# Optimization experiments

Measured on AMD Instinct MI355X. Metric: run time of the kernel, lower is better.

Reference implementation:

```python
import jax, jax.numpy as jnp
import numpy as np
from jax import lax

# BatchNorm2d(affine=False) in eval mode with initial running stats (mean=0, var=1)
# reduces to a constant scale. (Original torch module in train mode would use batch
# stats of the dispatched subset; we use the eval-mode form for a deterministic,
# vectorizable reference.)
BN_SCALE = 1.0 / np.sqrt(1.0 + 1e-5)
DN = ('NCHW', 'OIHW', 'NCHW')


def _dw(x, w, pad, dil=1):
    # depthwise conv, kernel [C,1,k,k]
    return lax.conv_general_dilated(x, w, (1, 1), [(pad, pad), (pad, pad)],
                                    rhs_dilation=(dil, dil), dimension_numbers=DN,
                                    feature_group_count=x.shape[1])


def _pw(x, w):
    # pointwise 1x1 conv, kernel [C,C,1,1]
    return lax.conv_general_dilated(x, w, (1, 1), 'VALID', dimension_numbers=DN)


def _sep(x, d1, p1, d2, p2, pad):
    # DARTS SepConv: (ReLU-dw-pw-BN) x 2
    y = _pw(_dw(jax.nn.relu(x), d1, pad), p1) * BN_SCALE
    return _pw(_dw(jax.nn.relu(y), d2, pad), p2) * BN_SCALE


def _dil(x, d, p, pad):
    # DARTS DilConv: ReLU-dw(dilation=2)-pw-BN
    return _pw(_dw(jax.nn.relu(x), d, pad, 2), p) * BN_SCALE


def _maxpool3(x):
    y = jnp.pad(x, ((0, 0), (0, 0), (1, 1), (1, 1)), constant_values=-jnp.inf)
    return lax.reduce_window(y, -jnp.inf, lax.max, (1, 1, 3, 3), (1, 1, 1, 1), 'VALID')


def _avgpool3(x):
    # avg_pool 3x3 stride 1 pad 1, count_include_pad=False
    pad = [(0, 0), (0, 0), (1, 1), (1, 1)]
    s = lax.reduce_window(x, 0.0, lax.add, (1, 1, 3, 3), (1, 1, 1, 1), pad)
    c = lax.reduce_window(jnp.ones_like(x), 0.0, lax.add, (1, 1, 3, 3), (1, 1, 1, 1), pad)
    return s / c


def _mixed_forward(x, weights, params, top):
    B, n_op = weights.shape
    _, idx = lax.top_k(weights, top)                    # [B, top]
    sel = jax.nn.one_hot(idx, n_op).sum(axis=1) > 0     # [B, n_op] bool: op in top-k
    # softmax over logits masked to -inf outside top-k => non-selected ops weight 0
    gate = jax.nn.softmax(jnp.where(sel, weights, -jnp.inf), axis=-1)  # [B, n_op]
    (sc3_d1, sc3_p1, sc3_d2, sc3_p2,
     sc5_d1, sc5_p1, sc5_d2, sc5_p2,
     dc3_d, dc3_p, dc5_d, dc5_p) = params
    # PRIMITIVES order: none, max_pool_3x3, avg_pool_3x3, skip_connect,
    # sep_conv_3x3, sep_conv_5x5, dil_conv_3x3, dil_conv_5x5
    op_outs = [
        None,                        # 'none' contributes zeros
        _maxpool3(x) * BN_SCALE,     # pool ops are followed by BN(affine=False)
        _avgpool3(x) * BN_SCALE,
        x,                           # skip_connect (stride=1 -> Identity)
        _sep(x, sc3_d1, sc3_p1, sc3_d2, sc3_p2, 1),
        _sep(x, sc5_d1, sc5_p1, sc5_d2, sc5_p2, 2),
        _dil(x, dc3_d, dc3_p, 2),
        _dil(x, dc5_d, dc5_p, 4),
    ]
    out = jnp.zeros_like(x)
    for i, y in enumerate(op_outs):
        if y is not None:
            out = out + gate[:, i, None, None, None] * y
    return out, weights  # second output is gate_value_cp (clone of gate input)


def setup_inputs():
    key = jax.random.key(0)
    ks = jax.random.split(key, 16)
    B, C, H, W = 64, 128, 32, 32
    def p(k, shape):
        return jax.random.normal(k, shape, jnp.float32) * 0.05
    return {
        'x': jax.random.normal(ks[0], (B, C, H, W), jnp.float32),
        'weights': jax.random.normal(ks[1], (B, 8), jnp.float32),
        'sc3_d1': p(ks[2], (C, 1, 3, 3)), 'sc3_p1': p(ks[3], (C, C, 1, 1)),
        'sc3_d2': p(ks[4], (C, 1, 3, 3)), 'sc3_p2': p(ks[5], (C, C, 1, 1)),
        'sc5_d1': p(ks[6], (C, 1, 5, 5)), 'sc5_p1': p(ks[7], (C, C, 1, 1)),
        'sc5_d2': p(ks[8], (C, 1, 5, 5)), 'sc5_p2': p(ks[9], (C, C, 1, 1)),
        'dc3_d': p(ks[10], (C, 1, 3, 3)), 'dc3_p': p(ks[11], (C, C, 1, 1)),
        'dc5_d': p(ks[12], (C, 1, 5, 5)), 'dc5_p': p(ks[13], (C, C, 1, 1)),
        'top': 2,
    }


def reference(x, weights, sc3_d1, sc3_p1, sc3_d2, sc3_p2, sc5_d1, sc5_p1, sc5_d2, sc5_p2, dc3_d, dc3_p, dc5_d, dc5_p, top):
    params = (sc3_d1, sc3_p1, sc3_d2, sc3_p2, sc5_d1, sc5_p1, sc5_d2, sc5_p2,
              dc3_d, dc3_p, dc5_d, dc5_p)
    return _mixed_forward(x, weights, params, top)
```

## Files before the change

### kernel.cpp

```cpp
#include <hip/hip_runtime.h>
#include <hip/hip_bf16.h>


#define BN_SCALE 0.9999950000374997f
#define BB 64
#define CC 128
#define HH 32
#define WW 32
#define PLANE (HH*WW)
#define SAMP (CC*PLANE)
#define NOUT0 (BB*SAMP)
#define LROW 136

typedef __attribute__((ext_vector_type(8))) short bf16x8;
typedef __attribute__((ext_vector_type(4))) float f32x4;

__device__ __forceinline__ float us2f(unsigned int u) {
    unsigned int x = (u & 0xffffu) << 16;
    float f; __builtin_memcpy(&f, &x, 4); return f;
}
__device__ __forceinline__ unsigned short f2us(float f) {
    __hip_bfloat16 h = __float2bfloat16(f);
    unsigned short u; __builtin_memcpy(&u, &h, 2); return u;
}

__global__ void k_gates(const float* __restrict__ wlog,
                        const void* __restrict__ topp,
                        float* __restrict__ gates,
                        int* __restrict__ cnum, int* __restrict__ cops,
                        float* __restrict__ out_w) {
    int b = threadIdx.x;

    int top = -1;
    {
        unsigned int u0 = *(const unsigned int*)topp;
        int i32 = (int)u0;
        if (i32 >= 1 && i32 <= 8) top = i32;
        else {
            float f32; __builtin_memcpy(&f32, &u0, 4);
            if (f32 >= 1.f && f32 <= 8.f) top = (int)(f32 + 0.5f);
            else { float fb = us2f(u0); if (fb >= 1.f && fb <= 8.f) top = (int)(fb + 0.5f); }
        }
        if (top < 1 || top > 8) top = 2;
    }

    float lw[8];
    #pragma unroll
    for (int i = 0; i < 8; ++i) {
        lw[i] = wlog[b * 8 + i];
        out_w[b * 8 + i] = lw[i];
    }
    bool sel[8] = {false,false,false,false,false,false,false,false};
    for (int t = 0; t < top; ++t) {
        int best = -1; float bv = -3.4e38f;
        #pragma unroll
        for (int i = 0; i < 8; ++i)
            if (!sel[i] && lw[i] > bv) { bv = lw[i]; best = i; }
        if (best >= 0) sel[best] = true;
    }
    float m = -3.4e38f;
    #pragma unroll
    for (int i = 0; i < 8; ++i) if (sel[i] && lw[i] > m) m = lw[i];
    float s = 0.f, e[8];
    #pragma unroll
    for (int i = 0; i < 8; ++i) { e[i] = sel[i] ? expf(lw[i] - m) : 0.f; s += e[i]; }
    float inv = (s > 0.f) ? 1.f / s : 0.f;
    float g[8];
    #pragma unroll
    for (int i = 0; i < 8; ++i) {
        g[i] = (s > 0.f) ? e[i] * inv : (sel[i] ? 1.f / (float)top : 0.f);
        gates[b * 8 + i] = g[i];
    }
    int n = 0;
    #pragma unroll
    for (int i = 4; i < 8; ++i)
        if (g[i] > 0.f) { if (n < 4) cops[b * 4 + n] = i; ++n; }
    cnum[b] = (n < 4) ? n : 4;
}

__global__ __launch_bounds__(256) void
k_pools(const float* __restrict__ x,
        const float* __restrict__ gates,
        float* __restrict__ out) {
    int plane = blockIdx.x;
    int b = plane >> 7;
    float g1 = gates[b * 8 + 1] * BN_SCALE;
    float g2 = gates[b * 8 + 2] * BN_SCALE;
    float g3 = gates[b * 8 + 3];
    float* op = out + (size_t)plane * PLANE;
    if (g1 == 0.f && g2 == 0.f && g3 == 0.f) {
        ((float4*)op)[threadIdx.x] = make_float4(0.f, 0.f, 0.f, 0.f);
        return;
    }
    __shared__ float sx[PLANE];
    ((float4*)sx)[threadIdx.x] = ((const float4*)(x + (size_t)plane * PLANE))[threadIdx.x];
    __syncthreads();
    #pragma unroll
    for (int j = 0; j < 4; ++j) {
        int px = threadIdx.x + j * 256;
        int h = px >> 5, w = px & 31;
        float mx = -3.4e38f, sm = 0.f;
        int cnt = 0;
        #pragma unroll
        for (int dh = -1; dh <= 1; ++dh) {
            int ih = h + dh;
            if ((unsigned)ih >= HH) continue;
            #pragma unroll
            for (int dw = -1; dw <= 1; ++dw) {
                int iw = w + dw;
                if ((unsigned)iw >= WW) continue;
                float v = sx[ih * WW + iw];
                mx = fmaxf(mx, v);
                sm += v;
                ++cnt;
            }
        }
        op[px] = g1 * mx + g2 * (sm / (float)cnt) + g3 * sx[px];
    }
}

template <int K, int DIL>
__device__ __forceinline__ void dw_comp(const float* __restrict__ sx,
                                        const float* __restrict__ wd, int c,
                                        unsigned short* __restrict__ opp) {
    constexpr int PAD = (K / 2) * DIL;
    float wk[K * K];
    #pragma unroll
    for (int i = 0; i < K * K; ++i) wk[i] = wd[c * K * K + i];
    #pragma unroll
    for (int j = 0; j < 4; ++j) {
        int px = threadIdx.x + j * 256;
        int h = px >> 5, w = px & 31;
        float acc = 0.f;
        #pragma unroll
        for (int ky = 0; ky < K; ++ky) {
            int ih = h + ky * DIL - PAD;
            if ((unsigned)ih >= HH) continue;
            #pragma unroll
            for (int kx = 0; kx < K; ++kx) {
                int iw = w + kx * DIL - PAD;
                if ((unsigned)iw >= WW) continue;
                acc = fmaf(wk[ky * K + kx], sx[ih * WW + iw], acc);
            }
        }
        opp[px] = f2us(acc);
    }
}

__global__ __launch_bounds__(256) void
k_dw_first(const float* __restrict__ x,
           const float* __restrict__ w4, const float* __restrict__ w5,
           const float* __restrict__ w6, const float* __restrict__ w7,
           const float* __restrict__ gates,
           unsigned short* __restrict__ A4, unsigned short* __restrict__ A5,
           unsigned short* __restrict__ P6, unsigned short* __restrict__ P7) {
    int plane = blockIdx.x;
    int b = plane >> 7, c = plane & 127;
    float g4 = gates[b * 8 + 4], g5 = gates[b * 8 + 5];
    float g6 = gates[b * 8 + 6], g7 = gates[b * 8 + 7];
    if (g4 == 0.f && g5 == 0.f && g6 == 0.f && g7 == 0.f) return;
    __shared__ float sx[PLANE];
    {
        float4 v = ((const float4*)(x + (size_t)plane * PLANE))[threadIdx.x];
        ((float4*)sx)[threadIdx.x] =
            make_float4(fmaxf(v.x, 0.f), fmaxf(v.y, 0.f),
                        fmaxf(v.z, 0.f), fmaxf(v.w, 0.f));
    }
    __syncthreads();
    size_t off = (size_t)plane * PLANE;
    if (g4 != 0.f) dw_comp<3, 1>(sx, w4, c, A4 + off);
    if (g5 != 0.f) dw_comp<5, 1>(sx, w5, c, A5 + off);
    if (g6 != 0.f) dw_comp<3, 2>(sx, w6, c, P6 + off);
    if (g7 != 0.f) dw_comp<5, 2>(sx, w7, c, P7 + off);
}

__global__ __launch_bounds__(256) void
k_dw_second(const unsigned short* __restrict__ B4,
            const unsigned short* __restrict__ B5,
            const float* __restrict__ w4, const float* __restrict__ w5,
            const float* __restrict__ gates,
            unsigned short* __restrict__ P4, unsigned short* __restrict__ P5) {
    int plane = blockIdx.x;
    int b = plane >> 7, c = plane & 127;
    float g4 = gates[b * 8 + 4], g5 = gates[b * 8 + 5];
    if (g4 == 0.f && g5 == 0.f) return;
    __shared__ float sx[PLANE];
    size_t off = (size_t)plane * PLANE;
    if (g4 != 0.f) {
        ushort4 v = ((const ushort4*)(B4 + off))[threadIdx.x];
        ((float4*)sx)[threadIdx.x] =
            make_float4(fmaxf(us2f(v.x), 0.f), fmaxf(us2f(v.y), 0.f),
                        fmaxf(us2f(v.z), 0.f), fmaxf(us2f(v.w), 0.f));
        __syncthreads();
        dw_comp<3, 1>(sx, w4, c, P4 + off);
        __syncthreads();
    }
    if (g5 != 0.f) {
        ushort4 v = ((const ushort4*)(B5 + off))[threadIdx.x];
        ((float4*)sx)[threadIdx.x] =
            make_float4(fmaxf(us2f(v.x), 0.f), fmaxf(us2f(v.y), 0.f),
                        fmaxf(us2f(v.z), 0.f), fmaxf(us2f(v.w), 0.f));
        __syncthreads();
        dw_comp<5, 1>(sx, w5, c, P5 + off);
    }
}


__device__ __forceinline__ void stage_wt(unsigned short* __restrict__ Wt,
                                         const float* __restrict__ W,
                                         int co0, float s) {
    unsigned int* Wtu = (unsigned int*)Wt;
    #pragma unroll
    for (int i = 0; i < 16; ++i) {
        int idx = threadIdx.x + i * 256;
        int r = idx >> 6, c2 = idx & 63;
        float2 v = *(const float2*)(W + (size_t)(co0 + r) * CC + c2 * 2);
        Wtu[r * (LROW / 2) + c2] =
            (unsigned int)f2us(v.x * s) | ((unsigned int)f2us(v.y * s) << 16);
    }
}

__device__ __forceinline__ void stage_bt(unsigned short* __restrict__ Bt,
                                         const unsigned short* __restrict__ ib,
                                         int hw0) {
    #pragma unroll
    for (int i = 0; i < 16; ++i) {
        int idx = threadIdx.x + i * 256;
        int ci = idx >> 5, hp = (idx & 31) * 2;
        unsigned int raw = *(const unsigned int*)(ib + (size_t)ci * PLANE + hw0 + hp);
        Bt[hp * LROW + ci]       = (unsigned short)(raw & 0xffffu);
        Bt[(hp + 1) * LROW + ci] = (unsigned short)(raw >> 16);
    }
}

__device__ __forceinline__ void mfma_tile(const unsigned short* __restrict__ Wt,
                                          const unsigned short* __restrict__ Bt,
                                          int wave, int quad, int m,
                                          f32x4 acc[4]) {
    #pragma unroll
    for (int kb = 0; kb < 4; ++kb) {
        int cio = kb * 32 + quad * 8;
        bf16x8 a = *(const bf16x8*)(Wt + (wave * 16 + m) * LROW + cio);
        #pragma unroll
        for (int nt = 0; nt < 4; ++nt) {
            bf16x8 bv = *(const bf16x8*)(Bt + (nt * 16 + m) * LROW + cio);
            acc[nt] = __builtin_amdgcn_mfma_f32_16x16x32_bf16(a, bv, acc[nt], 0, 0, 0);
        }
    }
}

__global__ __launch_bounds__(256) void
k_pw_mid(const unsigned short* __restrict__ A4,
         const unsigned short* __restrict__ A5,
         const float* __restrict__ W4, const float* __restrict__ W5,
         const float* __restrict__ gates,
         unsigned short* __restrict__ B4, unsigned short* __restrict__ B5) {
    int blk = blockIdx.x;
    int hwt = blk & 15;
    int coh = (blk >> 4) & 1;
    int b = blk >> 5;
    float g4 = gates[b * 8 + 4], g5 = gates[b * 8 + 5];
    if (g4 == 0.f && g5 == 0.f) return;
    int co0 = coh * 64, hw0 = hwt * 64;
    int wave = threadIdx.x >> 6, lane = threadIdx.x & 63;
    int quad = lane >> 4, m = lane & 15;
    __shared__ unsigned short Wt[64 * LROW];
    __shared__ unsigned short Bt[64 * LROW];
    bool staged = false;
    #pragma unroll
    for (int opi = 0; opi < 2; ++opi) {
        if ((opi ? g5 : g4) == 0.f) continue;
        if (staged) __syncthreads();
        stage_wt(Wt, opi ? W5 : W4, co0, BN_SCALE);
        stage_bt(Bt, (opi ? A5 : A4) + (size_t)b * SAMP, hw0);
        __syncthreads();
        f32x4 acc[4];
        #pragma unroll
        for (int i = 0; i < 4; ++i) acc[i] = (f32x4){0.f, 0.f, 0.f, 0.f};
        mfma_tile(Wt, Bt, wave, quad, m, acc);
        unsigned short* ob = opi ? B5 : B4;
        #pragma unroll
        for (int nt = 0; nt < 4; ++nt)
            #pragma unroll
            for (int r = 0; r < 4; ++r) {
                int co = co0 + wave * 16 + quad * 4 + r;
                int col = hw0 + nt * 16 + m;
                ob[(size_t)(b * CC + co) * PLANE + col] = f2us(acc[nt][r]);
            }
        staged = true;
    }
}

__global__ __launch_bounds__(256) void
k_pw_final(const unsigned short* __restrict__ P4,
           const unsigned short* __restrict__ P5,
           const unsigned short* __restrict__ P6,
           const unsigned short* __restrict__ P7,
           const float* __restrict__ W4, const float* __restrict__ W5,
           const float* __restrict__ W6, const float* __restrict__ W7,
           const float* __restrict__ gates,
           const int* __restrict__ cnum, const int* __restrict__ cops,
           float* __restrict__ out) {
    int blk = blockIdx.x;
    int hwt = blk & 15;
    int coh = (blk >> 4) & 1;
    int b = blk >> 5;
    int n = cnum[b];
    if (n == 0) return;
    int co0 = coh * 64, hw0 = hwt * 64;
    int wave = threadIdx.x >> 6, lane = threadIdx.x & 63;
    int quad = lane >> 4, m = lane & 15;
    __shared__ unsigned short Wt[64 * LROW];
    __shared__ unsigned short Bt[64 * LROW];
    f32x4 acc[4];
    #pragma unroll
    for (int i = 0; i < 4; ++i) acc[i] = (f32x4){0.f, 0.f, 0.f, 0.f};
    for (int t = 0; t < n; ++t) {
        int op = cops[b * 4 + t];
        float gs = gates[b * 8 + op] * BN_SCALE;
        const unsigned short* src;
        const float* W;
        switch (op) {
            case 4:  src = P4; W = W4; break;
            case 5:  src = P5; W = W5; break;
            case 6:  src = P6; W = W6; break;
            default: src = P7; W = W7; break;
        }
        if (t) __syncthreads();
        stage_wt(Wt, W, co0, gs);
        stage_bt(Bt, src + (size_t)b * SAMP, hw0);
        __syncthreads();
        mfma_tile(Wt, Bt, wave, quad, m, acc);
    }
    #pragma unroll
    for (int nt = 0; nt < 4; ++nt)
        #pragma unroll
        for (int r = 0; r < 4; ++r) {
            int co = co0 + wave * 16 + quad * 4 + r;
            int col = hw0 + nt * 16 + m;
            size_t idx = (size_t)(b * CC + co) * PLANE + col;
            out[idx] += acc[nt][r];
        }
}

extern "C" void kernel_launch(void* const* d_in, const int* in_sizes, int n_in,
                              void* d_out, int out_size, void* d_ws, size_t ws_size,
                              hipStream_t stream) {
    const float* x      = (const float*)d_in[0];
    const float* wlog   = (const float*)d_in[1];
    const float* sc3_d1 = (const float*)d_in[2];
    const float* sc3_p1 = (const float*)d_in[3];
    const float* sc3_d2 = (const float*)d_in[4];
    const float* sc3_p2 = (const float*)d_in[5];
    const float* sc5_d1 = (const float*)d_in[6];
    const float* sc5_p1 = (const float*)d_in[7];
    const float* sc5_d2 = (const float*)d_in[8];
    const float* sc5_p2 = (const float*)d_in[9];
    const float* dc3_d  = (const float*)d_in[10];
    const float* dc3_p  = (const float*)d_in[11];
    const float* dc5_d  = (const float*)d_in[12];
    const float* dc5_p  = (const float*)d_in[13];
    const void* topp    = d_in[14];

    float* out  = (float*)d_out;
    float* outw = out + NOUT0;

    float* gates = (float*)d_ws;
    int*   cnum  = (int*)((char*)d_ws + 2048);
    int*   cops  = (int*)((char*)d_ws + 2304);
    unsigned short* base = (unsigned short*)((char*)d_ws + 4096);
    unsigned short* A4 = base;
    unsigned short* A5 = base + (size_t)NOUT0;
    unsigned short* B4 = base + (size_t)NOUT0 * 2;
    unsigned short* B5 = base + (size_t)NOUT0 * 3;
    unsigned short* P4 = base + (size_t)NOUT0 * 4;
    unsigned short* P5 = base + (size_t)NOUT0 * 5;
    unsigned short* P6 = base + (size_t)NOUT0 * 6;
    unsigned short* P7 = base + (size_t)NOUT0 * 7;

    k_gates<<<1, 64, 0, stream>>>(wlog, topp, gates, cnum, cops, outw);
    k_pools<<<BB * CC, 256, 0, stream>>>(x, gates, out);
    k_dw_first<<<BB * CC, 256, 0, stream>>>(x, sc3_d1, sc5_d1, dc3_d, dc5_d,
                                            gates, A4, A5, P6, P7);
    k_pw_mid<<<BB * 32, 256, 0, stream>>>(A4, A5, sc3_p1, sc5_p1, gates, B4, B5);
    k_dw_second<<<BB * CC, 256, 0, stream>>>(B4, B5, sc3_d2, sc5_d2, gates, P4, P5);
    k_pw_final<<<BB * 32, 256, 0, stream>>>(P4, P5, P6, P7,
                                            sc3_p2, sc5_p2, dc3_p, dc5_p,
                                            gates, cnum, cops, out);
}
```

Measured before the change: 196.9 us.

## Pre-convert pointwise weights to bf16 and restructure pointwise GEMM tiling

Adds a prep kernel that converts all six pointwise weight matrices to bf16 once, with BN scaling folded in, instead of every block converting weights into shared memory. The pointwise kernels now read weight fragments directly from global/L2 and stage only the activation tile, with the gate scale applied to activations. k_pw_mid splits blocks by op rather than by output-channel half, and k_pw_final gives each block all 128 output channels, so activations are staged once per tile and output writes become vectorized. The cost is more accumulator registers per thread and repeated uncached global weight reads from every block.

```diff
diff --git a/kernel.cpp b/kernel.cpp
--- a/kernel.cpp
+++ b/kernel.cpp
@@ -10,7 +10,6 @@
 #define PLANE (HH*WW)
 #define SAMP (CC*PLANE)
 #define NOUT0 (BB*SAMP)
-#define LROW 136
 
 typedef __attribute__((ext_vector_type(8))) short bf16x8;
 typedef __attribute__((ext_vector_type(4))) float f32x4;
@@ -76,6 +75,25 @@
     for (int i = 4; i < 8; ++i)
         if (g[i] > 0.f) { if (n < 4) cops[b * 4 + n] = i; ++n; }
     cnum[b] = (n < 4) ? n : 4;
+}
+
+__global__ __launch_bounds__(256) void
+k_prep(const float* __restrict__ w0, const float* __restrict__ w1,
+       const float* __restrict__ w2, const float* __restrict__ w3,
+       const float* __restrict__ w4, const float* __restrict__ w5,
+       unsigned short* __restrict__ Wbf) {
+    int idx = blockIdx.x * 256 + threadIdx.x;
+    int mat = idx >> 14, e = idx & 16383;
+    const float* src; float s = 1.f;
+    switch (mat) {
+        case 0:  src = w0; s = BN_SCALE; break;
+        case 1:  src = w1; s = BN_SCALE; break;
+        case 2:  src = w2; break;
+        case 3:  src = w3; break;
+        case 4:  src = w4; break;
+        default: src = w5; break;
+    }
+    Wbf[idx] = f2us(src[e] * s);
 }
 
 __global__ __launch_bounds__(256) void
@@ -206,88 +224,68 @@
 }
 
 
-__device__ __forceinline__ void stage_wt(unsigned short* __restrict__ Wt,
-                                         const float* __restrict__ W,
-                                         int co0, float s) {
-    unsigned int* Wtu = (unsigned int*)Wt;
+__device__ __forceinline__ void stage_bt(unsigned int* __restrict__ BtU,
+                                         const unsigned short* __restrict__ A,
+                                         int hw0, float s) {
+    unsigned short* Bs = (unsigned short*)BtU;
     #pragma unroll
     for (int i = 0; i < 16; ++i) {
         int idx = threadIdx.x + i * 256;
-        int r = idx >> 6, c2 = idx & 63;
-        float2 v = *(const float2*)(W + (size_t)(co0 + r) * CC + c2 * 2);
-        Wtu[r * (LROW / 2) + c2] =
-            (unsigned int)f2us(v.x * s) | ((unsigned int)f2us(v.y * s) << 16);
-    }
-}
-
-__device__ __forceinline__ void stage_bt(unsigned short* __restrict__ Bt,
-                                         const unsigned short* __restrict__ ib,
-                                         int hw0) {
-    #pragma unroll
-    for (int i = 0; i < 16; ++i) {
-        int idx = threadIdx.x + i * 256;
-        int ci = idx >> 5, hp = (idx & 31) * 2;
-        unsigned int raw = *(const unsigned int*)(ib + (size_t)ci * PLANE + hw0 + hp);
-        Bt[hp * LROW + ci]       = (unsigned short)(raw & 0xffffu);
-        Bt[(hp + 1) * LROW + ci] = (unsigned short)(raw >> 16);
-    }
-}
-
-__device__ __forceinline__ void mfma_tile(const unsigned short* __restrict__ Wt,
-                                          const unsigned short* __restrict__ Bt,
-                                          int wave, int quad, int m,
-                                          f32x4 acc[4]) {
-    #pragma unroll
-    for (int kb = 0; kb < 4; ++kb) {
-        int cio = kb * 32 + quad * 8;
-        bf16x8 a = *(const bf16x8*)(Wt + (wave * 16 + m) * LROW + cio);
-        #pragma unroll
-        for (int nt = 0; nt < 4; ++nt) {
-            bf16x8 bv = *(const bf16x8*)(Bt + (nt * 16 + m) * LROW + cio);
-            acc[nt] = __builtin_amdgcn_mfma_f32_16x16x32_bf16(a, bv, acc[nt], 0, 0, 0);
-        }
-    }
+        int ci = idx >> 5, p = idx & 31;
+        unsigned int raw = *(const unsigned int*)(A + (size_t)ci * PLANE + hw0 + 2 * p);
+        Bs[(2 * p) * 130 + ci]     = f2us(us2f(raw) * s);
+        Bs[(2 * p + 1) * 130 + ci] = f2us(us2f(raw >> 16) * s);
+    }
+}
+
+__device__ __forceinline__ bf16x8 afrag(const unsigned int* __restrict__ BtU,
+                                        int r, int ko2) {
+    union { unsigned int u[4]; bf16x8 v; } f;
+    #pragma unroll
+    for (int j = 0; j < 4; ++j) f.u[j] = BtU[r * 65 + ko2 + j];
+    return f.v;
 }
 
 __global__ __launch_bounds__(256) void
 k_pw_mid(const unsigned short* __restrict__ A4,
          const unsigned short* __restrict__ A5,
-         const float* __restrict__ W4, const float* __restrict__ W5,
+         const unsigned short* __restrict__ Wbf,
          const float* __restrict__ gates,
          unsigned short* __restrict__ B4, unsigned short* __restrict__ B5) {
     int blk = blockIdx.x;
     int hwt = blk & 15;
-    int coh = (blk >> 4) & 1;
+    int opi = (blk >> 4) & 1;
     int b = blk >> 5;
-    float g4 = gates[b * 8 + 4], g5 = gates[b * 8 + 5];
-    if (g4 == 0.f && g5 == 0.f) return;
-    int co0 = coh * 64, hw0 = hwt * 64;
+    if (gates[b * 8 + 4 + opi] == 0.f) return;
+    int hw0 = hwt * 64;
     int wave = threadIdx.x >> 6, lane = threadIdx.x & 63;
-    int quad = lane >> 4, m = lane & 15;
-    __shared__ unsigned short Wt[64 * LROW];
-    __shared__ unsigned short Bt[64 * LROW];
-    bool staged = false;
-    #pragma unroll
-    for (int opi = 0; opi < 2; ++opi) {
-        if ((opi ? g5 : g4) == 0.f) continue;
-        if (staged) __syncthreads();
-        stage_wt(Wt, opi ? W5 : W4, co0, BN_SCALE);
-        stage_bt(Bt, (opi ? A5 : A4) + (size_t)b * SAMP, hw0);
-        __syncthreads();
-        f32x4 acc[4];
-        #pragma unroll
-        for (int i = 0; i < 4; ++i) acc[i] = (f32x4){0.f, 0.f, 0.f, 0.f};
-        mfma_tile(Wt, Bt, wave, quad, m, acc);
-        unsigned short* ob = opi ? B5 : B4;
-        #pragma unroll
-        for (int nt = 0; nt < 4; ++nt)
-            #pragma unroll
-            for (int r = 0; r < 4; ++r) {
-                int co = co0 + wave * 16 + quad * 4 + r;
-                int col = hw0 + nt * 16 + m;
-                ob[(size_t)(b * CC + co) * PLANE + col] = f2us(acc[nt][r]);
-            }
-        staged = true;
+    int q = lane >> 4, mm = lane & 15;
+    int r = wave * 16 + mm;
+    __shared__ unsigned int BtU[64 * 65];
+    stage_bt(BtU, (opi ? A5 : A4) + (size_t)b * SAMP, hw0, 1.f);
+    __syncthreads();
+    const unsigned short* Wb = Wbf + opi * 16384;
+    f32x4 acc[8];
+    #pragma unroll
+    for (int i = 0; i < 8; ++i) acc[i] = (f32x4){0.f, 0.f, 0.f, 0.f};
+    #pragma unroll
+    for (int kb = 0; kb < 4; ++kb) {
+        bf16x8 a = afrag(BtU, r, kb * 16 + q * 4);
+        #pragma unroll
+        for (int nt = 0; nt < 8; ++nt) {
+            bf16x8 bv = *(const bf16x8*)(Wb + (nt * 16 + mm) * CC + kb * 32 + q * 8);
+            acc[nt] = __builtin_amdgcn_mfma_f32_16x16x32_bf16(a, bv, acc[nt], 0, 0, 0);
+        }
+    }
+    unsigned short* ob = (opi ? B5 : B4) + (size_t)b * SAMP;
+    int hwbase = hw0 + wave * 16 + q * 4;
+    #pragma unroll
+    for (int nt = 0; nt < 8; ++nt) {
+        int co = nt * 16 + mm;
+        uint2 pk;
+        pk.x = (unsigned int)f2us(acc[nt][0]) | ((unsigned int)f2us(acc[nt][1]) << 16);
+        pk.y = (unsigned int)f2us(acc[nt][2]) | ((unsigned int)f2us(acc[nt][3]) << 16);
+        *(uint2*)(ob + (size_t)co * PLANE + hwbase) = pk;
     }
 }
 
@@ -296,51 +294,57 @@
            const unsigned short* __restrict__ P5,
            const unsigned short* __restrict__ P6,
            const unsigned short* __restrict__ P7,
-           const float* __restrict__ W4, const float* __restrict__ W5,
-           const float* __restrict__ W6, const float* __restrict__ W7,
+           const unsigned short* __restrict__ Wbf,
            const float* __restrict__ gates,
            const int* __restrict__ cnum, const int* __restrict__ cops,
            float* __restrict__ out) {
     int blk = blockIdx.x;
     int hwt = blk & 15;
-    int coh = (blk >> 4) & 1;
-    int b = blk >> 5;
+    int b = blk >> 4;
     int n = cnum[b];
     if (n == 0) return;
-    int co0 = coh * 64, hw0 = hwt * 64;
+    int hw0 = hwt * 64;
     int wave = threadIdx.x >> 6, lane = threadIdx.x & 63;
-    int quad = lane >> 4, m = lane & 15;
-    __shared__ unsigned short Wt[64 * LROW];
-    __shared__ unsigned short Bt[64 * LROW];
-    f32x4 acc[4];
-    #pragma unroll
-    for (int i = 0; i < 4; ++i) acc[i] = (f32x4){0.f, 0.f, 0.f, 0.f};
+    int q = lane >> 4, mm = lane & 15;
+    int r = wave * 16 + mm;
+    __shared__ unsigned int BtU[64 * 65];
+    f32x4 acc[8];
+    #pragma unroll
+    for (int i = 0; i < 8; ++i) acc[i] = (f32x4){0.f, 0.f, 0.f, 0.f};
     for (int t = 0; t < n; ++t) {
         int op = cops[b * 4 + t];
         float gs = gates[b * 8 + op] * BN_SCALE;
         const unsigned short* src;
-        const float* W;
         switch (op) {
-            case 4:  src = P4; W = W4; break;
-            case 5:  src = P5; W = W5; break;
-            case 6:  src = P6; W = W6; break;
-            default: src = P7; W = W7; break;
+            case 4:  src = P4; break;
+            case 5:  src = P5; break;
+            case 6:  src = P6; break;
+            default: src = P7; break;
         }
         if (t) __syncthreads();
-        stage_wt(Wt, W, co0, gs);
-        stage_bt(Bt, src + (size_t)b * SAMP, hw0);
+        stage_bt(BtU, src + (size_t)b * SAMP, hw0, gs);
         __syncthreads();
-        mfma_tile(Wt, Bt, wave, quad, m, acc);
-    }
-    #pragma unroll
-    for (int nt = 0; nt < 4; ++nt)
-        #pragma unroll
-        for (int r = 0; r < 4; ++r) {
-            int co = co0 + wave * 16 + quad * 4 + r;
-            int col = hw0 + nt * 16 + m;
-            size_t idx = (size_t)(b * CC + co) * PLANE + col;
-            out[idx] += acc[nt][r];
-        }
+        const unsigned short* Wb = Wbf + (op - 2) * 16384;
+        #pragma unroll
+        for (int kb = 0; kb < 4; ++kb) {
+            bf16x8 a = afrag(BtU, r, kb * 16 + q * 4);
+            #pragma unroll
+            for (int nt = 0; nt < 8; ++nt) {
+                bf16x8 bv = *(const bf16x8*)(Wb + (nt * 16 + mm) * CC + kb * 32 + q * 8);
+                acc[nt] = __builtin_amdgcn_mfma_f32_16x16x32_bf16(a, bv, acc[nt], 0, 0, 0);
+            }
+        }
+    }
+    int hwbase = hw0 + wave * 16 + q * 4;
+    #pragma unroll
+    for (int nt = 0; nt < 8; ++nt) {
+        int co = nt * 16 + mm;
+        float* p = out + (size_t)(b * CC + co) * PLANE + hwbase;
+        float4 o = *(float4*)p;
+        o.x += acc[nt][0]; o.y += acc[nt][1];
+        o.z += acc[nt][2]; o.w += acc[nt][3];
+        *(float4*)p = o;
+    }
 }
 
 extern "C" void kernel_launch(void* const* d_in, const int* in_sizes, int n_in,
@@ -368,7 +372,8 @@
     float* gates = (float*)d_ws;
     int*   cnum  = (int*)((char*)d_ws + 2048);
     int*   cops  = (int*)((char*)d_ws + 2304);
-    unsigned short* base = (unsigned short*)((char*)d_ws + 4096);
+    unsigned short* Wbf  = (unsigned short*)((char*)d_ws + 4096);
+    unsigned short* base = (unsigned short*)((char*)d_ws + 200704);
     unsigned short* A4 = base;
     unsigned short* A5 = base + (size_t)NOUT0;
     unsigned short* B4 = base + (size_t)NOUT0 * 2;
@@ -379,12 +384,12 @@
     unsigned short* P7 = base + (size_t)NOUT0 * 7;
 
     k_gates<<<1, 64, 0, stream>>>(wlog, topp, gates, cnum, cops, outw);
+    k_prep<<<384, 256, 0, stream>>>(sc3_p1, sc5_p1, sc3_p2, sc5_p2, dc3_p, dc5_p, Wbf);
     k_pools<<<BB * CC, 256, 0, stream>>>(x, gates, out);
     k_dw_first<<<BB * CC, 256, 0, stream>>>(x, sc3_d1, sc5_d1, dc3_d, dc5_d,
                                             gates, A4, A5, P6, P7);
-    k_pw_mid<<<BB * 32, 256, 0, stream>>>(A4, A5, sc3_p1, sc5_p1, gates, B4, B5);
+    k_pw_mid<<<BB * 32, 256, 0, stream>>>(A4, A5, Wbf, gates, B4, B5);
     k_dw_second<<<BB * CC, 256, 0, stream>>>(B4, B5, sc3_d2, sc5_d2, gates, P4, P5);
-    k_pw_final<<<BB * 32, 256, 0, stream>>>(P4, P5, P6, P7,
-                                            sc3_p2, sc5_p2, dc3_p, dc5_p,
+    k_pw_final<<<BB * 16, 256, 0, stream>>>(P4, P5, P6, P7, Wbf,
                                             gates, cnum, cops, out);
 }
```

Result: slower. 202.6 us (+2.9%).
